# Performance work log

Hardware: AMD Instinct MI355X
Metric: run time of the kernel (lower is better)

The kernel has to match this reference:

```python
import jax, jax.numpy as jnp
import numpy as np

MARGIN = 0.1
WEIGHT_BCE = 1.0
WEIGHT_SIM = 1.0
B, L = 8192, 1024


def setup_inputs() -> dict:
    key = jax.random.key(0)
    k1, k2, k3, k4 = jax.random.split(key, 4)
    # scores must be valid probabilities for BCELoss
    scores = jax.random.uniform(k1, (B, L), dtype=jnp.float32, minval=1e-4, maxval=1.0 - 1e-4)
    candidate_lengths = jax.random.randint(k2, (B,), 1, L + 1)  # int, >=1
    # exactly one positive label per sample, at a random valid index
    pos_idx = (jax.random.uniform(k3, (B,)) * candidate_lengths.astype(jnp.float32)).astype(jnp.int32)
    labels = jnp.zeros((B, L), dtype=jnp.float32).at[jnp.arange(B), pos_idx].set(1.0)
    similarity_top_cand = jax.random.normal(k4, (B,), dtype=jnp.float32)
    return {
        "scores": scores,
        "candidate_lengths": candidate_lengths,
        "labels": labels,
        "similarity_top_cand": similarity_top_cand,
    }


def reference(scores, candidate_lengths, labels, similarity_top_cand):
    max_cand_len = scores.shape[1]
    idx = jnp.arange(max_cand_len)
    mask = (idx[None, :] < candidate_lengths[:, None])  # [B, L] bool
    maskf = mask.astype(scores.dtype)

    # ---- BinaryCELoss (torch BCELoss clamps log at -100) ----
    log_p = jnp.clip(jnp.log(scores), -100.0)
    log_1mp = jnp.clip(jnp.log1p(-scores), -100.0)
    bce_el = -(labels * log_p + (1.0 - labels) * log_1mp)  # [B, L]
    # faithful to original: .mean(1) then divided again by mask.sum(1)
    bce_per = (bce_el * maskf).mean(axis=1) / maskf.sum(axis=1)
    bce_loss = bce_per.mean()

    # ---- HingeRankLoss (vectorized; one positive per sample assumption) ----
    pos_mask = maskf * (labels == 1.0)
    neg_mask = maskf * (labels == 0.0)
    pos_sum = pos_mask.sum(axis=1)              # number of positives in valid range
    neg_cnt = neg_mask.sum(axis=1)
    # chosen score: the (single) positive's score, else -margin if no positive
    chosen = jnp.where(pos_sum > 0, (scores * pos_mask).sum(axis=1), -MARGIN)  # [B]
    hinge_el = jnp.maximum(MARGIN + scores - chosen[:, None], 0.0) * neg_mask   # [B, L]
    valid = (candidate_lengths > 0) & (neg_cnt > 0)
    per_sample = jnp.where(valid, hinge_el.sum(axis=1) / jnp.maximum(neg_cnt, 1.0), 0.0)
    vcnt = valid.sum().astype(scores.dtype)
    hinge_loss = jnp.where(vcnt > 0, per_sample.sum() / jnp.maximum(vcnt, 1.0), 0.0)

    # ---- similarity loss ----
    sim_loss = -similarity_top_cand.mean()

    combined = hinge_loss + WEIGHT_BCE * bce_loss + WEIGHT_SIM * sim_loss
    return (combined, hinge_loss, bce_loss, sim_loss)
```

## Files before the change

kernel.cpp:

```cpp
#include <hip/hip_runtime.h>

#define MARGIN 0.1f

__device__ __forceinline__ float wave_sum(float v) {
    #pragma unroll
    for (int o = 32; o > 0; o >>= 1) v += __shfl_down(v, o, 64);
    return v;
}

__global__ __launch_bounds__(256) void row_kernel(
    const float* __restrict__ scores,
    const int*   __restrict__ lens,
    const float* __restrict__ labels,
    const float* __restrict__ sim,
    float4* __restrict__ ws_part)
{
    const int lane = threadIdx.x & 63;
    const int wave = threadIdx.x >> 6;
    const int row  = blockIdx.x * 4 + wave;
    const int len  = lens[row];

    const float4* srow = reinterpret_cast<const float4*>(scores + (size_t)row * 1024);
    const float4* lrow = reinterpret_cast<const float4*>(labels + (size_t)row * 1024);

    float sv[16], lv[16];
    #pragma unroll
    for (int k = 0; k < 4; ++k) {
        const float4 s4 = srow[k * 64 + lane];
        const float4 l4 = lrow[k * 64 + lane];
        sv[k*4+0] = s4.x; sv[k*4+1] = s4.y; sv[k*4+2] = s4.z; sv[k*4+3] = s4.w;
        lv[k*4+0] = l4.x; lv[k*4+1] = l4.y; lv[k*4+2] = l4.z; lv[k*4+3] = l4.w;
    }

    float bce = 0.f, pos_sum = 0.f;
    #pragma unroll
    for (int k = 0; k < 4; ++k) {
        #pragma unroll
        for (int j = 0; j < 4; ++j) {
            const int   idx = (k * 64 + lane) * 4 + j;
            const float m   = (idx < len) ? 1.f : 0.f;
            const float s   = sv[k*4+j];
            const float lab = lv[k*4+j];
            const float arg = fmaf(lab, 2.f * s - 1.f, 1.f - s);
            bce     -= m * __logf(arg);
            pos_sum += m * lab * s;
        }
    }
    bce     = wave_sum(bce);
    pos_sum = wave_sum(pos_sum);
    pos_sum = __shfl(pos_sum, 0, 64);
    const float pc     = (pos_sum > 0.f) ? 1.f : 0.f;
    const float chosen = (pos_sum > 0.f) ? pos_sum : -MARGIN;
    const float nc     = (float)len - pc;

    float hinge = 0.f;
    #pragma unroll
    for (int k = 0; k < 4; ++k) {
        #pragma unroll
        for (int j = 0; j < 4; ++j) {
            const int   idx = (k * 64 + lane) * 4 + j;
            const float m   = (idx < len) ? 1.f : 0.f;
            hinge += m * (1.f - lv[k*4+j]) * fmaxf(MARGIN + sv[k*4+j] - chosen, 0.f);
        }
    }
    hinge = wave_sum(hinge);

    if (lane == 0) {
        const float bce_per = bce * (1.f / 1024.f) / (float)len;
        const bool  valid   = (len > 0) && (nc > 0.f);
        const float h_per   = valid ? hinge / fmaxf(nc, 1.f) : 0.f;
        ws_part[row] = make_float4(bce_per, h_per, valid ? 1.f : 0.f, sim[row]);
    }
}

__global__ __launch_bounds__(1024) void finalize_kernel(
    const float4* __restrict__ ws_part,
    float* __restrict__ out,
    int B)
{
    const int t    = threadIdx.x;
    const int lane = t & 63;
    const int wave = t >> 6;

    float b_acc = 0.f, h_acc = 0.f, v_acc = 0.f, s_acc = 0.f;
    for (int i = t; i < B; i += 1024) {
        const float4 p = ws_part[i];
        b_acc += p.x;
        h_acc += p.y;
        v_acc += p.z;
        s_acc += p.w;
    }
    b_acc = wave_sum(b_acc);
    h_acc = wave_sum(h_acc);
    v_acc = wave_sum(v_acc);
    s_acc = wave_sum(s_acc);

    __shared__ float red[4][16];
    if (lane == 0) {
        red[0][wave] = b_acc;
        red[1][wave] = h_acc;
        red[2][wave] = v_acc;
        red[3][wave] = s_acc;
    }
    __syncthreads();

    if (t == 0) {
        float b_tot = 0.f, h_tot = 0.f, v_tot = 0.f, s_tot = 0.f;
        #pragma unroll
        for (int w = 0; w < 16; ++w) {
            b_tot += red[0][w];
            h_tot += red[1][w];
            v_tot += red[2][w];
            s_tot += red[3][w];
        }
        const float bce_loss   = b_tot / (float)B;
        const float hinge_loss = (v_tot > 0.f) ? h_tot / fmaxf(v_tot, 1.f) : 0.f;
        const float sim_loss   = -s_tot / (float)B;

        out[0] = hinge_loss + bce_loss + sim_loss;
        out[1] = hinge_loss;
        out[2] = bce_loss;
        out[3] = sim_loss;
    }
}

extern "C" void kernel_launch(void* const* d_in, const int* in_sizes, int n_in,
                              void* d_out, int out_size, void* d_ws, size_t ws_size,
                              hipStream_t stream) {
    const float* scores = (const float*)d_in[0];
    const int*   lens   = (const int*)d_in[1];
    const float* labels = (const float*)d_in[2];
    const float* sim    = (const float*)d_in[3];
    float* out = (float*)d_out;

    const int B = in_sizes[1];

    float4* ws_part = (float4*)d_ws;

    row_kernel<<<B / 4, 256, 0, stream>>>(scores, lens, labels, sim, ws_part);
    finalize_kernel<<<1, 1024, 0, stream>>>(ws_part, out, B);
}
```

Before: 99.89 us.

## Fuse row and finalize kernels with grid-stride loop and last-block reduction

Replaces the two-kernel scheme with one persistent kernel of 512 blocks, each wave looping over rows and accumulating partial sums in registers. Each block writes one set of partials, and the last block to arrive, found with an atomic counter, performs the final reduction. This removes the second launch and the per-row workspace traffic. The cost is fewer in-flight rows per wave with a serial row loop, and a global counter that must reset correctly between calls.

```diff
diff --git a/kernel.cpp b/kernel.cpp
--- a/kernel.cpp
+++ b/kernel.cpp
@@ -1,6 +1,9 @@
 #include <hip/hip_runtime.h>
 
 #define MARGIN 0.1f
+#define NBLK   512
+
+__device__ int g_counter = 0;
 
 __device__ __forceinline__ float wave_sum(float v) {
     #pragma unroll
@@ -8,125 +11,141 @@
     return v;
 }
 
-__global__ __launch_bounds__(256) void row_kernel(
+__global__ __launch_bounds__(256) void fused_kernel(
     const float* __restrict__ scores,
     const int*   __restrict__ lens,
     const float* __restrict__ labels,
     const float* __restrict__ sim,
-    float4* __restrict__ ws_part)
+    float* __restrict__ ws_part,
+    float* __restrict__ out,
+    int B)
 {
     const int lane = threadIdx.x & 63;
     const int wave = threadIdx.x >> 6;
-    const int row  = blockIdx.x * 4 + wave;
-    const int len  = lens[row];
+    const int gw   = blockIdx.x * 4 + wave;
+    const int nw   = NBLK * 4;
 
-    const float4* srow = reinterpret_cast<const float4*>(scores + (size_t)row * 1024);
-    const float4* lrow = reinterpret_cast<const float4*>(labels + (size_t)row * 1024);
+    float b_acc = 0.f, h_acc = 0.f, v_acc = 0.f, s_acc = 0.f;
 
-    float sv[16], lv[16];
-    #pragma unroll
-    for (int k = 0; k < 4; ++k) {
-        const float4 s4 = srow[k * 64 + lane];
-        const float4 l4 = lrow[k * 64 + lane];
-        sv[k*4+0] = s4.x; sv[k*4+1] = s4.y; sv[k*4+2] = s4.z; sv[k*4+3] = s4.w;
-        lv[k*4+0] = l4.x; lv[k*4+1] = l4.y; lv[k*4+2] = l4.z; lv[k*4+3] = l4.w;
+    for (int row = gw; row < B; row += nw) {
+        const int len = lens[row];
+        const float4* srow = reinterpret_cast<const float4*>(scores + (size_t)row * 1024);
+        const float4* lrow = reinterpret_cast<const float4*>(labels + (size_t)row * 1024);
+
+        float sv[16], lv[16];
+        #pragma unroll
+        for (int k = 0; k < 4; ++k) {
+            const float4 s4 = srow[k * 64 + lane];
+            const float4 l4 = lrow[k * 64 + lane];
+            sv[k*4+0] = s4.x; sv[k*4+1] = s4.y; sv[k*4+2] = s4.z; sv[k*4+3] = s4.w;
+            lv[k*4+0] = l4.x; lv[k*4+1] = l4.y; lv[k*4+2] = l4.z; lv[k*4+3] = l4.w;
+        }
+
+        float bce = 0.f, pos_sum = 0.f;
+        #pragma unroll
+        for (int k = 0; k < 4; ++k) {
+            #pragma unroll
+            for (int j = 0; j < 4; ++j) {
+                const int   idx = (k * 64 + lane) * 4 + j;
+                const float m   = (idx < len) ? 1.f : 0.f;
+                const float s   = sv[k*4+j];
+                const float lab = lv[k*4+j];
+                const float arg = fmaf(lab, 2.f * s - 1.f, 1.f - s);
+                bce     -= m * __logf(arg);
+                pos_sum += m * lab * s;
+            }
+        }
+        bce     = wave_sum(bce);
+        pos_sum = wave_sum(pos_sum);
+        pos_sum = __shfl(pos_sum, 0, 64);
+        const float pc     = (pos_sum > 0.f) ? 1.f : 0.f;
+        const float chosen = (pos_sum > 0.f) ? pos_sum : -MARGIN;
+        const float nc     = (float)len - pc;
+
+        float hinge = 0.f;
+        #pragma unroll
+        for (int k = 0; k < 4; ++k) {
+            #pragma unroll
+            for (int j = 0; j < 4; ++j) {
+                const int   idx = (k * 64 + lane) * 4 + j;
+                const float m   = (idx < len) ? 1.f : 0.f;
+                hinge += m * (1.f - lv[k*4+j]) * fmaxf(MARGIN + sv[k*4+j] - chosen, 0.f);
+            }
+        }
+        hinge = wave_sum(hinge);
+
+        const bool valid = (len > 0) && (nc > 0.f);
+        b_acc += bce * (1.f / 1024.f) / (float)len;
+        h_acc += valid ? hinge / fmaxf(nc, 1.f) : 0.f;
+        v_acc += valid ? 1.f : 0.f;
+        s_acc += sim[row];
     }
 
-    float bce = 0.f, pos_sum = 0.f;
-    #pragma unroll
-    for (int k = 0; k < 4; ++k) {
-        #pragma unroll
-        for (int j = 0; j < 4; ++j) {
-            const int   idx = (k * 64 + lane) * 4 + j;
-            const float m   = (idx < len) ? 1.f : 0.f;
-            const float s   = sv[k*4+j];
-            const float lab = lv[k*4+j];
-            const float arg = fmaf(lab, 2.f * s - 1.f, 1.f - s);
-            bce     -= m * __logf(arg);
-            pos_sum += m * lab * s;
-        }
-    }
-    bce     = wave_sum(bce);
-    pos_sum = wave_sum(pos_sum);
-    pos_sum = __shfl(pos_sum, 0, 64);
-    const float pc     = (pos_sum > 0.f) ? 1.f : 0.f;
-    const float chosen = (pos_sum > 0.f) ? pos_sum : -MARGIN;
-    const float nc     = (float)len - pc;
-
-    float hinge = 0.f;
-    #pragma unroll
-    for (int k = 0; k < 4; ++k) {
-        #pragma unroll
-        for (int j = 0; j < 4; ++j) {
-            const int   idx = (k * 64 + lane) * 4 + j;
-            const float m   = (idx < len) ? 1.f : 0.f;
-            hinge += m * (1.f - lv[k*4+j]) * fmaxf(MARGIN + sv[k*4+j] - chosen, 0.f);
-        }
-    }
-    hinge = wave_sum(hinge);
-
+    __shared__ float red[4][4];
+    __shared__ int   amLast;
+    if (threadIdx.x == 0) amLast = 0;
     if (lane == 0) {
-        const float bce_per = bce * (1.f / 1024.f) / (float)len;
-        const bool  valid   = (len > 0) && (nc > 0.f);
-        const float h_per   = valid ? hinge / fmaxf(nc, 1.f) : 0.f;
-        ws_part[row] = make_float4(bce_per, h_per, valid ? 1.f : 0.f, sim[row]);
-    }
-}
-
-__global__ __launch_bounds__(1024) void finalize_kernel(
-    const float4* __restrict__ ws_part,
-    float* __restrict__ out,
-    int B)
-{
-    const int t    = threadIdx.x;
-    const int lane = t & 63;
-    const int wave = t >> 6;
-
-    float b_acc = 0.f, h_acc = 0.f, v_acc = 0.f, s_acc = 0.f;
-    for (int i = t; i < B; i += 1024) {
-        const float4 p = ws_part[i];
-        b_acc += p.x;
-        h_acc += p.y;
-        v_acc += p.z;
-        s_acc += p.w;
-    }
-    b_acc = wave_sum(b_acc);
-    h_acc = wave_sum(h_acc);
-    v_acc = wave_sum(v_acc);
-    s_acc = wave_sum(s_acc);
-
-    __shared__ float red[4][16];
-    if (lane == 0) {
-        red[0][wave] = b_acc;
-        red[1][wave] = h_acc;
-        red[2][wave] = v_acc;
-        red[3][wave] = s_acc;
+        red[wave][0] = b_acc;
+        red[wave][1] = h_acc;
+        red[wave][2] = v_acc;
+        red[wave][3] = s_acc;
     }
     __syncthreads();
 
-    if (t == 0) {
-        float b_tot = 0.f, h_tot = 0.f, v_tot = 0.f, s_tot = 0.f;
-        #pragma unroll
-        for (int w = 0; w < 16; ++w) {
-            b_tot += red[0][w];
-            h_tot += red[1][w];
-            v_tot += red[2][w];
-            s_tot += red[3][w];
+    if (threadIdx.x == 0) {
+        const float b = red[0][0] + red[1][0] + red[2][0] + red[3][0];
+        const float h = red[0][1] + red[1][1] + red[2][1] + red[3][1];
+        const float v = red[0][2] + red[1][2] + red[2][2] + red[3][2];
+        const float s = red[0][3] + red[1][3] + red[2][3] + red[3][3];
+        __hip_atomic_store(&ws_part[blockIdx.x*4+0], b, __ATOMIC_RELAXED, __HIP_MEMORY_SCOPE_AGENT);
+        __hip_atomic_store(&ws_part[blockIdx.x*4+1], h, __ATOMIC_RELAXED, __HIP_MEMORY_SCOPE_AGENT);
+        __hip_atomic_store(&ws_part[blockIdx.x*4+2], v, __ATOMIC_RELAXED, __HIP_MEMORY_SCOPE_AGENT);
+        __hip_atomic_store(&ws_part[blockIdx.x*4+3], s, __ATOMIC_RELAXED, __HIP_MEMORY_SCOPE_AGENT);
+        const int old = __hip_atomic_fetch_add(&g_counter, 1, __ATOMIC_ACQ_REL, __HIP_MEMORY_SCOPE_AGENT);
+        if (old == NBLK - 1) amLast = 1;
+    }
+    __syncthreads();
+
+    if (amLast) {
+        float b = 0.f, h = 0.f, v = 0.f, s = 0.f;
+        for (int p = threadIdx.x; p < NBLK; p += 256) {
+            b += __hip_atomic_load(&ws_part[p*4+0], __ATOMIC_RELAXED, __HIP_MEMORY_SCOPE_AGENT);
+            h += __hip_atomic_load(&ws_part[p*4+1], __ATOMIC_RELAXED, __HIP_MEMORY_SCOPE_AGENT);
+            v += __hip_atomic_load(&ws_part[p*4+2], __ATOMIC_RELAXED, __HIP_MEMORY_SCOPE_AGENT);
+            s += __hip_atomic_load(&ws_part[p*4+3], __ATOMIC_RELAXED, __HIP_MEMORY_SCOPE_AGENT);
         }
-        const float bce_loss   = b_tot / (float)B;
-        const float hinge_loss = (v_tot > 0.f) ? h_tot / fmaxf(v_tot, 1.f) : 0.f;
-        const float sim_loss   = -s_tot / (float)B;
-
-        out[0] = hinge_loss + bce_loss + sim_loss;
-        out[1] = hinge_loss;
-        out[2] = bce_loss;
-        out[3] = sim_loss;
+        b = wave_sum(b);
+        h = wave_sum(h);
+        v = wave_sum(v);
+        s = wave_sum(s);
+        if (lane == 0) {
+            red[wave][0] = b;
+            red[wave][1] = h;
+            red[wave][2] = v;
+            red[wave][3] = s;
+        }
+        __syncthreads();
+        if (threadIdx.x == 0) {
+            const float bt = red[0][0] + red[1][0] + red[2][0] + red[3][0];
+            const float ht = red[0][1] + red[1][1] + red[2][1] + red[3][1];
+            const float vt = red[0][2] + red[1][2] + red[2][2] + red[3][2];
+            const float st = red[0][3] + red[1][3] + red[2][3] + red[3][3];
+            const float bce_loss   = bt / (float)B;
+            const float hinge_loss = (vt > 0.f) ? ht / fmaxf(vt, 1.f) : 0.f;
+            const float sim_loss   = -st / (float)B;
+            out[0] = hinge_loss + bce_loss + sim_loss;
+            out[1] = hinge_loss;
+            out[2] = bce_loss;
+            out[3] = sim_loss;
+            __hip_atomic_store(&g_counter, 0, __ATOMIC_RELAXED, __HIP_MEMORY_SCOPE_AGENT);
+        }
     }
 }
 
 extern "C" void kernel_launch(void* const* d_in, const int* in_sizes, int n_in,
                               void* d_out, int out_size, void* d_ws, size_t ws_size,
                               hipStream_t stream) {
+    (void)n_in; (void)out_size; (void)ws_size;
     const float* scores = (const float*)d_in[0];
     const int*   lens   = (const int*)d_in[1];
     const float* labels = (const float*)d_in[2];
@@ -135,8 +154,6 @@
 
     const int B = in_sizes[1];
 
-    float4* ws_part = (float4*)d_ws;
-
-    row_kernel<<<B / 4, 256, 0, stream>>>(scores, lens, labels, sim, ws_part);
-    finalize_kernel<<<1, 1024, 0, stream>>>(ws_part, out, B);
+    fused_kernel<<<NBLK, 256, 0, stream>>>(scores, lens, labels, sim,
+                                           (float*)d_ws, out, B);
 }
```

Result: slower. 109.0 us (+9.1%).
